# Kernel tuning notes

Hardware: AMD Instinct MI355X
Metric: run time of the kernel (lower is better)

The kernel has to match this reference:

```python
import jax, jax.numpy as jnp
import numpy as np

B, S, F = 4, 2048, 512
H, DH, OUT = 8, 64, 512  # attention_dim=512 -> head_dim=64
NEG_SLOPE = 0.01


def setup_inputs() -> dict:
    key = jax.random.key(0)
    ks = jax.random.split(key, 9)
    sc_in = 1.0 / np.sqrt(F)
    sc_hd = 1.0 / np.sqrt(H * DH)
    return {
        "x": jax.random.normal(ks[0], (B, S, F), dtype=jnp.float32),
        "Wq": jax.random.normal(ks[1], (F, H, DH), dtype=jnp.float32) * sc_in,
        "bq": jnp.zeros((H, DH), dtype=jnp.float32),
        "Wk": jax.random.normal(ks[2], (F, H, DH), dtype=jnp.float32) * sc_in,
        "bk": jnp.zeros((H, DH), dtype=jnp.float32),
        "Wv": jax.random.normal(ks[3], (F, H, DH), dtype=jnp.float32) * sc_in,
        "bv": jnp.zeros((H, DH), dtype=jnp.float32),
        "Wo": jax.random.normal(ks[4], (H, DH, OUT), dtype=jnp.float32) * sc_hd,
        "bo": jnp.zeros((OUT,), dtype=jnp.float32),
    }


def reference(x, Wq, bq, Wk, bk, Wv, bv, Wo, bo):
    # QKV projections: DenseGeneral(axis=-1, features=(H, DH)) -> [B, S, H, DH]
    q = jnp.einsum('bsf,fhd->bshd', x, Wq) + bq
    k = jnp.einsum('bsf,fhd->bshd', x, Wk) + bk
    v = jnp.einsum('bsf,fhd->bshd', x, Wv) + bv

    # Pairwise squared L2: l2[b,h,i,j] = ||q[b,i,h]-k[b,j,h]||^2
    q2 = jnp.sum(q * q, axis=-1)              # [B, S, H]
    k2 = jnp.sum(k * k, axis=-1)              # [B, S, H]
    qk = jnp.einsum('bihd,bjhd->bhij', q, k)  # [B, H, S, S]
    l2 = (q2.transpose(0, 2, 1)[:, :, :, None]
          + k2.transpose(0, 2, 1)[:, :, None, :]
          - 2.0 * qk)

    # softmax over key axis j, then weights.T @ value (note the transpose:
    # output token index is j, summed over query index i, as in the original)
    w = jax.nn.softmax(-l2, axis=-1)                  # [B, H, Si, Sj]
    attn = jnp.einsum('bhij,bihd->bjhd', w, v)        # [B, S, H, DH]

    # out DenseGeneral contracting (H, DH)
    out = jnp.einsum('bshd,hdo->bso', attn, Wo) + bo
    return jnp.where(out >= 0, out, NEG_SLOPE * out)
```

## Files before the change

### kernel.cpp

```cpp
#include <hip/hip_runtime.h>


typedef __attribute__((ext_vector_type(8))) short bf16x8;
typedef __attribute__((ext_vector_type(4))) float f32x4;
typedef __attribute__((ext_vector_type(4))) unsigned short u16x4;

#define MFMA16 __builtin_amdgcn_mfma_f32_16x16x32_bf16
#define LOG2E 1.4426950408889634f
#define TWO_LOG2E 2.8853900817779268f

__device__ inline unsigned short f2bf(float f) {
  unsigned int u = __float_as_uint(f);
  unsigned int r = 0x7fffu + ((u >> 16) & 1u);
  return (unsigned short)((u + r) >> 16);
}
__device__ inline float bf2f(unsigned short h) {
  return __uint_as_float(((unsigned int)h) << 16);
}
__device__ inline float fexp2(float x) { return __builtin_amdgcn_exp2f(x); }

__device__ inline void gl_lds16(const unsigned short* g, unsigned short* lds) {
  __builtin_amdgcn_global_load_lds(
      (const __attribute__((address_space(1))) unsigned int*)g,
      (__attribute__((address_space(3))) unsigned int*)lds, 16, 0, 0);
}

#define NXB4 (8192*512/4)
#define NWQ (1536*512)
#define NWO (512*512)

__global__ __launch_bounds__(256) void prep(
    const float* __restrict__ x, const float* __restrict__ Wq,
    const float* __restrict__ Wk, const float* __restrict__ Wv,
    const float* __restrict__ Wo, const float* __restrict__ bq,
    const float* __restrict__ bk, const float* __restrict__ bv,
    unsigned short* __restrict__ xb, unsigned short* __restrict__ wqkvT,
    unsigned short* __restrict__ woT, float* __restrict__ biasp) {
  int i = blockIdx.x * blockDim.x + threadIdx.x;
  if (i < NXB4) {
    f32x4 v = ((const f32x4*)x)[i];
    u16x4 o;
    o.x = f2bf(v.x); o.y = f2bf(v.y); o.z = f2bf(v.z); o.w = f2bf(v.w);
    ((u16x4*)xb)[i] = o;
    return;
  }
  i -= NXB4;
  if (i < NWQ) {
    int n = i >> 9, f = i & 511;
    const float* W = (n < 512) ? Wq : (n < 1024) ? Wk : Wv;
    wqkvT[i] = f2bf(W[f * 512 + (n & 511)]);
    return;
  }
  i -= NWQ;
  if (i < NWO) {
    int o = i >> 9, hd = i & 511;
    woT[i] = f2bf(Wo[hd * 512 + o]);
    return;
  }
  i -= NWO;
  if (i < 1536) {
    biasp[i] = (i < 512) ? bq[i] : (i < 1024) ? bk[i - 512] : bv[i - 1024];
  }
}

template<int MODE>
__global__ __launch_bounds__(256) void gemm_bt(
    const unsigned short* __restrict__ A, const unsigned short* __restrict__ Bt,
    const float* __restrict__ bias,
    unsigned short* __restrict__ o_q, unsigned short* __restrict__ o_k,
    unsigned short* __restrict__ o_v, float* __restrict__ o_f, int K) {
  const int m0 = blockIdx.y * 128;
  const int n0 = blockIdx.x * 128;
  const int tid = threadIdx.x;
  const int w = tid >> 6, l = tid & 63, lg = l >> 4, ll = l & 15;
  const int wr = w >> 1, wc = w & 1;
  __shared__ unsigned short a_lds[128 * 32];
  __shared__ unsigned short b_lds[128 * 32];
  f32x4 acc[4][4] = {};
  const int nkt = K >> 5;
  for (int kt = 0; kt < nkt; ++kt) {
#pragma unroll
    for (int c = 0; c < 2; ++c) {
      const int cc_base = c * 256 + w * 64;
      const int cc = cc_base + l;
      const int row = cc >> 2, cl = cc & 3;
      gl_lds16(A + (size_t)(m0 + row) * K + kt * 32 + cl * 8, a_lds + cc_base * 8);
      gl_lds16(Bt + (size_t)(n0 + row) * K + kt * 32 + cl * 8, b_lds + cc_base * 8);
    }
    __syncthreads();
    bf16x8 af[4], bfr[4];
#pragma unroll
    for (int mi = 0; mi < 4; ++mi)
      af[mi] = *(const bf16x8*)(a_lds + (wr * 64 + mi * 16 + ll) * 32 + lg * 8);
#pragma unroll
    for (int ni = 0; ni < 4; ++ni)
      bfr[ni] = *(const bf16x8*)(b_lds + (wc * 64 + ni * 16 + ll) * 32 + lg * 8);
#pragma unroll
    for (int mi = 0; mi < 4; ++mi)
#pragma unroll
      for (int ni = 0; ni < 4; ++ni)
        acc[mi][ni] = MFMA16(af[mi], bfr[ni], acc[mi][ni], 0, 0, 0);
    __syncthreads();
  }
#pragma unroll
  for (int mi = 0; mi < 4; ++mi)
#pragma unroll
    for (int ni = 0; ni < 4; ++ni) {
      const int col = n0 + wc * 64 + ni * 16 + ll;
      const float bb = bias[col];
#pragma unroll
      for (int r = 0; r < 4; ++r) {
        const int row = m0 + wr * 64 + mi * 16 + lg * 4 + r;
        float v = acc[mi][ni][r] + bb;
        if (MODE == 0) {
          const int which = col >> 9, h = (col >> 6) & 7, d = col & 63;
          const int b = row >> 11, s = row & 2047;
          if (which == 0) v *= TWO_LOG2E;
          const size_t idx = ((size_t)((b * 8 + h) * 2048 + s)) * 64 + d;
          (which == 0 ? o_q : which == 1 ? o_k : o_v)[idx] = f2bf(v);
        } else {
          v = v >= 0.f ? v : 0.01f * v;
          o_f[(size_t)row * 512 + col] = v;
        }
      }
    }
}

__global__ __launch_bounds__(256) void k2_kernel(const unsigned short* __restrict__ k_g,
                                                 float* __restrict__ k2l_g) {
  const int lane = threadIdx.x & 63;
  const int wid = (blockIdx.x * blockDim.x + threadIdx.x) >> 6;
  const int nw = (gridDim.x * blockDim.x) >> 6;
  for (int row = wid; row < 32 * 2048; row += nw) {
    float v = bf2f(k_g[(size_t)row * 64 + lane]);
    v *= v;
#pragma unroll
    for (int m = 1; m < 64; m <<= 1) v += __shfl_xor(v, m);
    if (lane == 0) k2l_g[row] = LOG2E * v;
  }
}

__global__ __launch_bounds__(256) void transpose_v(const unsigned short* __restrict__ v_g,
                                                   const float* __restrict__ invl_g,
                                                   unsigned short* __restrict__ vt_g) {
  const int bh = blockIdx.x >> 5, st = blockIdx.x & 31;
  const int s0 = st * 64;
  __shared__ unsigned short tile[64][72];
  const int t = threadIdx.x;
  {
    const int sl = t >> 2, cg = t & 3;
    const float sc = invl_g[bh * 2048 + s0 + sl];
    const unsigned short* src = v_g + ((size_t)(bh * 2048 + s0 + sl)) * 64 + cg * 16;
    bf16x8 v0 = *(const bf16x8*)(src);
    bf16x8 v1 = *(const bf16x8*)(src + 8);
#pragma unroll
    for (int e = 0; e < 8; ++e) tile[sl][cg * 16 + e] = f2bf(sc * bf2f((unsigned short)v0[e]));
#pragma unroll
    for (int e = 0; e < 8; ++e) tile[sl][cg * 16 + 8 + e] = f2bf(sc * bf2f((unsigned short)v1[e]));
  }
  __syncthreads();
  {
    const int dl = t >> 2, sg = t & 3;
    bf16x8 o0, o1;
#pragma unroll
    for (int e = 0; e < 8; ++e) o0[e] = (short)tile[sg * 16 + e][dl];
#pragma unroll
    for (int e = 0; e < 8; ++e) o1[e] = (short)tile[sg * 16 + 8 + e][dl];
    unsigned short* dst = vt_g + ((size_t)(bh * 64 + dl)) * 2048 + s0 + sg * 16;
    *(bf16x8*)dst = o0;
    *(bf16x8*)(dst + 8) = o1;
  }
}

__global__ __launch_bounds__(256) void pass1(const unsigned short* __restrict__ q_g,
                                             const unsigned short* __restrict__ k_g,
                                             const float* __restrict__ k2l_g,
                                             float* __restrict__ invl_g) {
  const int bh = blockIdx.x >> 4, ib = blockIdx.x & 15;
  const int i0 = ib * 128;
  const int tid = threadIdx.x, w = tid >> 6, l = tid & 63, lg = l >> 4, ll = l & 15;
  __shared__ unsigned short k_lds[64 * 64];
  __shared__ float k2_lds[64];
  const unsigned short* qrow = q_g + ((size_t)(bh * 2048 + i0 + w * 32 + ll)) * 64;
  const bf16x8 qa00 = *(const bf16x8*)(qrow + lg * 8);
  const bf16x8 qa01 = *(const bf16x8*)(qrow + 32 + lg * 8);
  const bf16x8 qa10 = *(const bf16x8*)(qrow + 1024 + lg * 8);
  const bf16x8 qa11 = *(const bf16x8*)(qrow + 1024 + 32 + lg * 8);
  float lrun0[4] = {0.f, 0.f, 0.f, 0.f};
  float lrun1[4] = {0.f, 0.f, 0.f, 0.f};
  for (int jt = 0; jt < 32; ++jt) {
    const int j0 = jt * 64;
#pragma unroll
    for (int c = 0; c < 2; ++c) {
      const int cc_base = c * 256 + w * 64;
      const int cc = cc_base + l;
      const int row = cc >> 3, cl = cc & 7;
      gl_lds16(k_g + ((size_t)(bh * 2048 + j0 + row)) * 64 + ((cl ^ (row & 7)) * 8),
               k_lds + cc_base * 8);
    }
    if (tid < 64) k2_lds[tid] = k2l_g[bh * 2048 + j0 + tid];
    __syncthreads();
#pragma unroll
    for (int nf = 0; nf < 4; ++nf) {
      const int jr = nf * 16 + ll;
      const unsigned short* kb = k_lds + jr * 64;
      const int sw = jr & 7;
      bf16x8 b0 = *(const bf16x8*)(kb + ((lg ^ sw) * 8));
      bf16x8 b1 = *(const bf16x8*)(kb + (((4 + lg) ^ sw) * 8));
      f32x4 sa0 = {};
      sa0 = MFMA16(qa00, b0, sa0, 0, 0, 0);
      sa0 = MFMA16(qa01, b1, sa0, 0, 0, 0);
      f32x4 sa1 = {};
      sa1 = MFMA16(qa10, b0, sa1, 0, 0, 0);
      sa1 = MFMA16(qa11, b1, sa1, 0, 0, 0);
      const float k2v = k2_lds[jr];
      lrun0[0] += fexp2(sa0[0] - k2v);
      lrun0[1] += fexp2(sa0[1] - k2v);
      lrun0[2] += fexp2(sa0[2] - k2v);
      lrun0[3] += fexp2(sa0[3] - k2v);
      lrun1[0] += fexp2(sa1[0] - k2v);
      lrun1[1] += fexp2(sa1[1] - k2v);
      lrun1[2] += fexp2(sa1[2] - k2v);
      lrun1[3] += fexp2(sa1[3] - k2v);
    }
    __syncthreads();
  }
#pragma unroll
  for (int r = 0; r < 4; ++r) {
    float t0 = lrun0[r], t1 = lrun1[r];
#pragma unroll
    for (int m = 1; m < 16; m <<= 1) { t0 += __shfl_xor(t0, m); t1 += __shfl_xor(t1, m); }
    if (ll == 0) {
      invl_g[bh * 2048 + i0 + w * 32 + lg * 4 + r] = 1.f / t0;
      invl_g[bh * 2048 + i0 + w * 32 + 16 + lg * 4 + r] = 1.f / t1;
    }
  }
}

__global__ __launch_bounds__(256) void pass2(const unsigned short* __restrict__ q_g,
                                             const unsigned short* __restrict__ k_g,
                                             const unsigned short* __restrict__ vt_g,
                                             const float* __restrict__ k2l_g,
                                             unsigned short* __restrict__ part0,
                                             unsigned short* __restrict__ part1) {
  const int bh = blockIdx.x >> 4, jb = blockIdx.x & 15;
  const int by = blockIdx.y;
  const int j0 = jb * 128;
  const int it0 = by << 4, it_end = it0 + 16;
  const int tid = threadIdx.x, w = tid >> 6, l = tid & 63, lg = l >> 4, ll = l & 15;
  __shared__ unsigned short q_lds[2][64 * 64];
  __shared__ unsigned short vt_lds[2][64 * 64];
  __shared__ unsigned short p_lds[128 * 64];
  const unsigned short* q_base = q_g + (size_t)bh * 2048 * 64;
  const unsigned short* vt_base = vt_g + (size_t)bh * 64 * 2048;
  const unsigned short* krow = k_g + ((size_t)(bh * 2048 + j0 + w * 32 + ll)) * 64;
  const bf16x8 ka00 = *(const bf16x8*)(krow + lg * 8);
  const bf16x8 ka01 = *(const bf16x8*)(krow + 32 + lg * 8);
  const bf16x8 ka10 = *(const bf16x8*)(krow + 1024 + lg * 8);
  const bf16x8 ka11 = *(const bf16x8*)(krow + 1024 + 32 + lg * 8);
  float k2v0[4], k2v1[4];
#pragma unroll
  for (int r = 0; r < 4; ++r) {
    k2v0[r] = k2l_g[bh * 2048 + j0 + w * 32 + lg * 4 + r];
    k2v1[r] = k2l_g[bh * 2048 + j0 + w * 32 + 16 + lg * 4 + r];
  }
  f32x4 oacc0[4] = {};
  f32x4 oacc1[4] = {};
#pragma unroll
  for (int c = 0; c < 2; ++c) {
    const int cc_base = c * 256 + w * 64;
    const int cc = cc_base + l;
    const int row = cc >> 3, cl = cc & 7;
    const int csw = (cl ^ (row & 7)) * 8;
    gl_lds16(q_base + (size_t)(it0 * 64 + row) * 64 + csw, &q_lds[0][cc_base * 8]);
    gl_lds16(vt_base + (size_t)row * 2048 + it0 * 64 + csw, &vt_lds[0][cc_base * 8]);
  }
  __syncthreads();
  for (int it = it0; it < it_end; ++it) {
    const int slot = it & 1;
    if (it + 1 < it_end) {
      const int i1 = (it + 1) * 64;
#pragma unroll
      for (int c = 0; c < 2; ++c) {
        const int cc_base = c * 256 + w * 64;
        const int cc = cc_base + l;
        const int row = cc >> 3, cl = cc & 7;
        const int csw = (cl ^ (row & 7)) * 8;
        gl_lds16(q_base + (size_t)(i1 + row) * 64 + csw, &q_lds[slot ^ 1][cc_base * 8]);
        gl_lds16(vt_base + (size_t)row * 2048 + i1 + csw, &vt_lds[slot ^ 1][cc_base * 8]);
      }
    }
#pragma unroll
    for (int nf = 0; nf < 4; ++nf) {
      const int ir = nf * 16 + ll;
      const unsigned short* qb = &q_lds[slot][ir * 64];
      const int sw = ir & 7;
      bf16x8 b0 = *(const bf16x8*)(qb + ((lg ^ sw) * 8));
      bf16x8 b1 = *(const bf16x8*)(qb + (((4 + lg) ^ sw) * 8));
      f32x4 sa0 = {};
      sa0 = MFMA16(ka00, b0, sa0, 0, 0, 0);
      sa0 = MFMA16(ka01, b1, sa0, 0, 0, 0);
      f32x4 sa1 = {};
      sa1 = MFMA16(ka10, b0, sa1, 0, 0, 0);
      sa1 = MFMA16(ka11, b1, sa1, 0, 0, 0);
#pragma unroll
      for (int r = 0; r < 4; ++r) {
        const float p0 = fexp2(sa0[r] - k2v0[r]);
        const float p1 = fexp2(sa1[r] - k2v1[r]);
        const int ja = w * 32 + lg * 4 + r;
        const int jb2 = ja + 16;
        p_lds[ja * 64 + (ir ^ ((ja & 7) << 3))] =
            (unsigned short)(__float_as_uint(p0) >> 16);
        p_lds[jb2 * 64 + (ir ^ ((jb2 & 7) << 3))] =
            (unsigned short)(__float_as_uint(p1) >> 16);
      }
    }
    {
      const int jr0 = w * 32 + ll;
      const int jr1 = jr0 + 16;
      const int swp = ll & 7;
      const unsigned short* pb0 = p_lds + jr0 * 64;
      const unsigned short* pb1 = p_lds + jr1 * 64;
      bf16x8 pa00 = *(const bf16x8*)(pb0 + ((lg ^ swp) * 8));
      bf16x8 pa01 = *(const bf16x8*)(pb0 + (((4 + lg) ^ swp) * 8));
      bf16x8 pa10 = *(const bf16x8*)(pb1 + ((lg ^ swp) * 8));
      bf16x8 pa11 = *(const bf16x8*)(pb1 + (((4 + lg) ^ swp) * 8));
#pragma unroll
      for (int nf = 0; nf < 4; ++nf) {
        const int dr = nf * 16 + ll;
        const unsigned short* vb = &vt_lds[slot][dr * 64];
        const int sw = dr & 7;
        bf16x8 v0 = *(const bf16x8*)(vb + ((lg ^ sw) * 8));
        bf16x8 v1 = *(const bf16x8*)(vb + (((4 + lg) ^ sw) * 8));
        oacc0[nf] = MFMA16(pa00, v0, oacc0[nf], 0, 0, 0);
        oacc0[nf] = MFMA16(pa01, v1, oacc0[nf], 0, 0, 0);
        oacc1[nf] = MFMA16(pa10, v0, oacc1[nf], 0, 0, 0);
        oacc1[nf] = MFMA16(pa11, v1, oacc1[nf], 0, 0, 0);
      }
    }
    __syncthreads();
  }
  unsigned short* po = by ? part1 : part0;
  const int b = bh >> 3, h2 = bh & 7;
#pragma unroll
  for (int nf = 0; nf < 4; ++nf) {
    const int d = nf * 16 + ll;
#pragma unroll
    for (int r = 0; r < 4; ++r) {
      const int j = j0 + w * 32 + lg * 4 + r;
      po[((size_t)(b * 2048 + j)) * 512 + h2 * 64 + d] = f2bf(oacc0[nf][r]);
      po[((size_t)(b * 2048 + j + 16)) * 512 + h2 * 64 + d] = f2bf(oacc1[nf][r]);
    }
  }
}

__global__ __launch_bounds__(256) void combine(unsigned short* __restrict__ p0,
                                               const unsigned short* __restrict__ p1) {
  const int i = blockIdx.x * blockDim.x + threadIdx.x;
  bf16x8 a = ((const bf16x8*)p0)[i];
  bf16x8 b = ((const bf16x8*)p1)[i];
  bf16x8 o;
#pragma unroll
  for (int e = 0; e < 8; ++e)
    o[e] = (short)f2bf(bf2f((unsigned short)a[e]) + bf2f((unsigned short)b[e]));
  ((bf16x8*)p0)[i] = o;
}

extern "C" void kernel_launch(void* const* d_in, const int* in_sizes, int n_in,
                              void* d_out, int out_size, void* d_ws, size_t ws_size,
                              hipStream_t stream) {
  const float* x  = (const float*)d_in[0];
  const float* Wq = (const float*)d_in[1];
  const float* bq = (const float*)d_in[2];
  const float* Wk = (const float*)d_in[3];
  const float* bk = (const float*)d_in[4];
  const float* Wv = (const float*)d_in[5];
  const float* bv = (const float*)d_in[6];
  const float* Wo = (const float*)d_in[7];
  const float* bo = (const float*)d_in[8];
  float* out = (float*)d_out;
  char* ws = (char*)d_ws;

  unsigned short* xb    = (unsigned short*)(ws);
  unsigned short* wqkvT = (unsigned short*)(ws + 8388608);
  unsigned short* woT   = (unsigned short*)(ws + 9961472);
  float*          biasp = (float*)         (ws + 10485760);
  unsigned short* q_g   = (unsigned short*)(ws + 10493952);
  unsigned short* k_g   = (unsigned short*)(ws + 18882560);
  unsigned short* v_g   = (unsigned short*)(ws + 27271168);
  unsigned short* vt_g  = (unsigned short*)(ws + 35659776);
  float*          k2_g  = (float*)         (ws + 44048384);
  float*          invl_g= (float*)         (ws + 44310528);
  unsigned short* attnb = (unsigned short*)(ws + 44572672);
  if (ws_size < (size_t)52961280) return;

  prep<<<8199, 256, 0, stream>>>(x, Wq, Wk, Wv, Wo, bq, bk, bv, xb, wqkvT, woT, biasp);
  gemm_bt<0><<<dim3(12, 64), 256, 0, stream>>>(xb, wqkvT, biasp, q_g, k_g, v_g, nullptr, 512);
  k2_kernel<<<1024, 256, 0, stream>>>(k_g, k2_g);
  pass1<<<512, 256, 0, stream>>>(q_g, k_g, k2_g, invl_g);
  transpose_v<<<1024, 256, 0, stream>>>(v_g, invl_g, vt_g);
  pass2<<<dim3(512, 2), 256, 0, stream>>>(q_g, k_g, vt_g, k2_g, attnb, xb);
  combine<<<2048, 256, 0, stream>>>(attnb, xb);
  gemm_bt<1><<<dim3(4, 64), 256, 0, stream>>>(attnb, woT, bo, nullptr, nullptr, nullptr, out, 512);
}
```

Measured before the change: 161.9 us.

## Split pass1 key loop across two blocks and drop pass2 double buffering

Pass1 now splits the key-tile loop into two halves using a second grid dimension. Each block writes partial softmax denominators, and a new small kernel sums them and takes the reciprocal. This doubles the block count to raise occupancy and parallelism, at the cost of an extra launch. Pass2 swaps its double-buffered Q/V^T LDS staging for a single buffer loaded and synced each iteration. That cuts LDS use, which may allow more resident blocks, but the load latency is no longer overlapped with compute.

New measurement: 168.2 us. 3.9% more time.

```diff
diff --git a/kernel.cpp b/kernel.cpp
--- a/kernel.cpp
+++ b/kernel.cpp
@@ -175,9 +175,12 @@
 __global__ __launch_bounds__(256) void pass1(const unsigned short* __restrict__ q_g,
                                              const unsigned short* __restrict__ k_g,
                                              const float* __restrict__ k2l_g,
-                                             float* __restrict__ invl_g) {
+                                             float* __restrict__ ps0,
+                                             float* __restrict__ ps1) {
   const int bh = blockIdx.x >> 4, ib = blockIdx.x & 15;
   const int i0 = ib * 128;
+  const int by = blockIdx.y;
+  const int jt0 = by << 4, jt_end = jt0 + 16;
   const int tid = threadIdx.x, w = tid >> 6, l = tid & 63, lg = l >> 4, ll = l & 15;
   __shared__ unsigned short k_lds[64 * 64];
   __shared__ float k2_lds[64];
@@ -188,7 +191,7 @@
   const bf16x8 qa11 = *(const bf16x8*)(qrow + 1024 + 32 + lg * 8);
   float lrun0[4] = {0.f, 0.f, 0.f, 0.f};
   float lrun1[4] = {0.f, 0.f, 0.f, 0.f};
-  for (int jt = 0; jt < 32; ++jt) {
+  for (int jt = jt0; jt < jt_end; ++jt) {
     const int j0 = jt * 64;
 #pragma unroll
     for (int c = 0; c < 2; ++c) {
@@ -225,16 +228,24 @@
     }
     __syncthreads();
   }
+  float* ps = by ? ps1 : ps0;
 #pragma unroll
   for (int r = 0; r < 4; ++r) {
     float t0 = lrun0[r], t1 = lrun1[r];
 #pragma unroll
     for (int m = 1; m < 16; m <<= 1) { t0 += __shfl_xor(t0, m); t1 += __shfl_xor(t1, m); }
     if (ll == 0) {
-      invl_g[bh * 2048 + i0 + w * 32 + lg * 4 + r] = 1.f / t0;
-      invl_g[bh * 2048 + i0 + w * 32 + 16 + lg * 4 + r] = 1.f / t1;
-    }
-  }
+      ps[bh * 2048 + i0 + w * 32 + lg * 4 + r] = t0;
+      ps[bh * 2048 + i0 + w * 32 + 16 + lg * 4 + r] = t1;
+    }
+  }
+}
+
+__global__ __launch_bounds__(256) void inv_combine(const float* __restrict__ a,
+                                                   const float* __restrict__ b,
+                                                   float* __restrict__ invl) {
+  const int i = blockIdx.x * blockDim.x + threadIdx.x;
+  invl[i] = 1.f / (a[i] + b[i]);
 }
 
 __global__ __launch_bounds__(256) void pass2(const unsigned short* __restrict__ q_g,
@@ -248,8 +259,8 @@
   const int j0 = jb * 128;
   const int it0 = by << 4, it_end = it0 + 16;
   const int tid = threadIdx.x, w = tid >> 6, l = tid & 63, lg = l >> 4, ll = l & 15;
-  __shared__ unsigned short q_lds[2][64 * 64];
-  __shared__ unsigned short vt_lds[2][64 * 64];
+  __shared__ unsigned short q_lds[64 * 64];
+  __shared__ unsigned short vt_lds[64 * 64];
   __shared__ unsigned short p_lds[128 * 64];
   const unsigned short* q_base = q_g + (size_t)bh * 2048 * 64;
   const unsigned short* vt_base = vt_g + (size_t)bh * 64 * 2048;
@@ -266,34 +277,22 @@
   }
   f32x4 oacc0[4] = {};
   f32x4 oacc1[4] = {};
-#pragma unroll
-  for (int c = 0; c < 2; ++c) {
-    const int cc_base = c * 256 + w * 64;
-    const int cc = cc_base + l;
-    const int row = cc >> 3, cl = cc & 7;
-    const int csw = (cl ^ (row & 7)) * 8;
-    gl_lds16(q_base + (size_t)(it0 * 64 + row) * 64 + csw, &q_lds[0][cc_base * 8]);
-    gl_lds16(vt_base + (size_t)row * 2048 + it0 * 64 + csw, &vt_lds[0][cc_base * 8]);
-  }
-  __syncthreads();
   for (int it = it0; it < it_end; ++it) {
-    const int slot = it & 1;
-    if (it + 1 < it_end) {
-      const int i1 = (it + 1) * 64;
-#pragma unroll
-      for (int c = 0; c < 2; ++c) {
-        const int cc_base = c * 256 + w * 64;
-        const int cc = cc_base + l;
-        const int row = cc >> 3, cl = cc & 7;
-        const int csw = (cl ^ (row & 7)) * 8;
-        gl_lds16(q_base + (size_t)(i1 + row) * 64 + csw, &q_lds[slot ^ 1][cc_base * 8]);
-        gl_lds16(vt_base + (size_t)row * 2048 + i1 + csw, &vt_lds[slot ^ 1][cc_base * 8]);
-      }
-    }
+    const int i1 = it * 64;
+#pragma unroll
+    for (int c = 0; c < 2; ++c) {
+      const int cc_base = c * 256 + w * 64;
+      const int cc = cc_base + l;
+      const int row = cc >> 3, cl = cc & 7;
+      const int csw = (cl ^ (row & 7)) * 8;
+      gl_lds16(q_base + (size_t)(i1 + row) * 64 + csw, q_lds + cc_base * 8);
+      gl_lds16(vt_base + (size_t)row * 2048 + i1 + csw, vt_lds + cc_base * 8);
+    }
+    __syncthreads();
 #pragma unroll
     for (int nf = 0; nf < 4; ++nf) {
       const int ir = nf * 16 + ll;
-      const unsigned short* qb = &q_lds[slot][ir * 64];
+      const unsigned short* qb = q_lds + ir * 64;
       const int sw = ir & 7;
       bf16x8 b0 = *(const bf16x8*)(qb + ((lg ^ sw) * 8));
       bf16x8 b1 = *(const bf16x8*)(qb + (((4 + lg) ^ sw) * 8));
@@ -328,7 +327,7 @@
 #pragma unroll
       for (int nf = 0; nf < 4; ++nf) {
         const int dr = nf * 16 + ll;
-        const unsigned short* vb = &vt_lds[slot][dr * 64];
+        const unsigned short* vb = vt_lds + dr * 64;
         const int sw = dr & 7;
         bf16x8 v0 = *(const bf16x8*)(vb + ((lg ^ sw) * 8));
         bf16x8 v1 = *(const bf16x8*)(vb + (((4 + lg) ^ sw) * 8));
@@ -382,6 +381,8 @@
   char* ws = (char*)d_ws;
 
   unsigned short* xb    = (unsigned short*)(ws);
+  float*          ps0   = (float*)         (ws);
+  float*          ps1   = (float*)         (ws + 262144);
   unsigned short* wqkvT = (unsigned short*)(ws + 8388608);
   unsigned short* woT   = (unsigned short*)(ws + 9961472);
   float*          biasp = (float*)         (ws + 10485760);
@@ -397,7 +398,8 @@
   prep<<<8199, 256, 0, stream>>>(x, Wq, Wk, Wv, Wo, bq, bk, bv, xb, wqkvT, woT, biasp);
   gemm_bt<0><<<dim3(12, 64), 256, 0, stream>>>(xb, wqkvT, biasp, q_g, k_g, v_g, nullptr, 512);
   k2_kernel<<<1024, 256, 0, stream>>>(k_g, k2_g);
-  pass1<<<512, 256, 0, stream>>>(q_g, k_g, k2_g, invl_g);
+  pass1<<<dim3(512, 2), 256, 0, stream>>>(q_g, k_g, k2_g, ps0, ps1);
+  inv_combine<<<256, 256, 0, stream>>>(ps0, ps1, invl_g);
   transpose_v<<<1024, 256, 0, stream>>>(v_g, invl_g, vt_g);
   pass2<<<dim3(512, 2), 256, 0, stream>>>(q_g, k_g, vt_g, k2_g, attnb, xb);
   combine<<<2048, 256, 0, stream>>>(attnb, xb);
```

## Split pass2 reduction three ways and remap block indices across heads

Applied to the files above, without the earlier changes.

pass2's query-axis reduction is now split across three blocks in y (11/11/10 tiles) instead of two, which raises the grid from 1024 to 1536 blocks to better fill the GPU's compute units. The third partial is written into the now-unused v_g buffer, and a three-input combine kernel sums the partials. Both pass1 and pass2 also remap blockIdx so that consecutive blocks fall on different batch-heads, which may change how cache traffic is spread. The costs are extra partial writes and reads and one more bf16 rounding step in the combine.

Result: no change. 159.3 us (-1.6%).

```diff
diff --git a/kernel.cpp b/kernel.cpp
--- a/kernel.cpp
+++ b/kernel.cpp
@@ -176,7 +176,9 @@
                                              const unsigned short* __restrict__ k_g,
                                              const float* __restrict__ k2l_g,
                                              float* __restrict__ invl_g) {
-  const int bh = blockIdx.x >> 4, ib = blockIdx.x & 15;
+  const int bx = blockIdx.x;
+  const int bh = (bx & 7) * 4 + ((bx >> 3) >> 4);
+  const int ib = (bx >> 3) & 15;
   const int i0 = ib * 128;
   const int tid = threadIdx.x, w = tid >> 6, l = tid & 63, lg = l >> 4, ll = l & 15;
   __shared__ unsigned short k_lds[64 * 64];
@@ -242,11 +244,15 @@
                                              const unsigned short* __restrict__ vt_g,
                                              const float* __restrict__ k2l_g,
                                              unsigned short* __restrict__ part0,
-                                             unsigned short* __restrict__ part1) {
-  const int bh = blockIdx.x >> 4, jb = blockIdx.x & 15;
+                                             unsigned short* __restrict__ part1,
+                                             unsigned short* __restrict__ part2) {
+  const int bx = blockIdx.x;
+  const int bh = (bx & 7) * 4 + ((bx >> 3) >> 4);
+  const int jb = (bx >> 3) & 15;
   const int by = blockIdx.y;
   const int j0 = jb * 128;
-  const int it0 = by << 4, it_end = it0 + 16;
+  const int it0 = by * 11;
+  const int it_end = (by == 2) ? 32 : it0 + 11;
   const int tid = threadIdx.x, w = tid >> 6, l = tid & 63, lg = l >> 4, ll = l & 15;
   __shared__ unsigned short q_lds[2][64 * 64];
   __shared__ unsigned short vt_lds[2][64 * 64];
@@ -266,14 +272,15 @@
   }
   f32x4 oacc0[4] = {};
   f32x4 oacc1[4] = {};
+  const int pslot = it0 & 1;
 #pragma unroll
   for (int c = 0; c < 2; ++c) {
     const int cc_base = c * 256 + w * 64;
     const int cc = cc_base + l;
     const int row = cc >> 3, cl = cc & 7;
     const int csw = (cl ^ (row & 7)) * 8;
-    gl_lds16(q_base + (size_t)(it0 * 64 + row) * 64 + csw, &q_lds[0][cc_base * 8]);
-    gl_lds16(vt_base + (size_t)row * 2048 + it0 * 64 + csw, &vt_lds[0][cc_base * 8]);
+    gl_lds16(q_base + (size_t)(it0 * 64 + row) * 64 + csw, &q_lds[pslot][cc_base * 8]);
+    gl_lds16(vt_base + (size_t)row * 2048 + it0 * 64 + csw, &vt_lds[pslot][cc_base * 8]);
   }
   __syncthreads();
   for (int it = it0; it < it_end; ++it) {
@@ -340,7 +347,7 @@
     }
     __syncthreads();
   }
-  unsigned short* po = by ? part1 : part0;
+  unsigned short* po = (by == 0) ? part0 : (by == 1) ? part1 : part2;
   const int b = bh >> 3, h2 = bh & 7;
 #pragma unroll
   for (int nf = 0; nf < 4; ++nf) {
@@ -354,15 +361,18 @@
   }
 }
 
-__global__ __launch_bounds__(256) void combine(unsigned short* __restrict__ p0,
-                                               const unsigned short* __restrict__ p1) {
+__global__ __launch_bounds__(256) void combine3(unsigned short* __restrict__ p0,
+                                                const unsigned short* __restrict__ p1,
+                                                const unsigned short* __restrict__ p2) {
   const int i = blockIdx.x * blockDim.x + threadIdx.x;
   bf16x8 a = ((const bf16x8*)p0)[i];
   bf16x8 b = ((const bf16x8*)p1)[i];
+  bf16x8 c = ((const bf16x8*)p2)[i];
   bf16x8 o;
 #pragma unroll
   for (int e = 0; e < 8; ++e)
-    o[e] = (short)f2bf(bf2f((unsigned short)a[e]) + bf2f((unsigned short)b[e]));
+    o[e] = (short)f2bf(bf2f((unsigned short)a[e]) + bf2f((unsigned short)b[e]) +
+                       bf2f((unsigned short)c[e]));
   ((bf16x8*)p0)[i] = o;
 }
 
@@ -399,7 +409,7 @@
   k2_kernel<<<1024, 256, 0, stream>>>(k_g, k2_g);
   pass1<<<512, 256, 0, stream>>>(q_g, k_g, k2_g, invl_g);
   transpose_v<<<1024, 256, 0, stream>>>(v_g, invl_g, vt_g);
-  pass2<<<dim3(512, 2), 256, 0, stream>>>(q_g, k_g, vt_g, k2_g, attnb, xb);
-  combine<<<2048, 256, 0, stream>>>(attnb, xb);
+  pass2<<<dim3(512, 3), 256, 0, stream>>>(q_g, k_g, vt_g, k2_g, attnb, xb, v_g);
+  combine3<<<2048, 256, 0, stream>>>(attnb, xb, v_g);
   gemm_bt<1><<<dim3(4, 64), 256, 0, stream>>>(attnb, woT, bo, nullptr, nullptr, nullptr, out, 512);
 }
```
